# Kernel optimization log

Measured on AMD Instinct MI355X. Metric: run time of the kernel, lower is better.

## Reference

```python
import jax, jax.numpy as jnp
import numpy as np

N = 256
BIG = 1e9  # acts as +inf for float32 duals


def solve_lap(C):
    """Exact linear assignment (min-cost) via Jonker-Volgenant shortest
    augmenting paths with dual potentials. Returns [n,n] 0/1 labelling with
    exactly one 1 per row and per column (same optimum as scipy's
    linear_sum_assignment, up to ties)."""
    n = C.shape[0]
    dt = C.dtype
    big = jnp.asarray(BIG, dt)
    # 1-indexed padded cost: row/col 0 are dummies
    C1 = jnp.zeros((n + 1, n + 1), dt).at[1:, 1:].set(C)

    def row_body(i, carry):
        u, v, p = carry  # u: row duals, v: col duals, p[j] = row matched to col j (0 = free)
        p = p.at[0].set(i)

        def cond(st):
            u, v, p, used, minv, way, j0 = st
            return p[j0] != 0

        def body(st):
            u, v, p, used, minv, way, j0 = st
            used = used.at[j0].set(True)
            i0 = p[j0]
            cur = C1[i0] - u[i0] - v            # reduced costs of row i0, all cols
            upd = (~used) & (cur < minv)
            minv = jnp.where(upd, cur, minv)
            way = jnp.where(upd, j0, way)
            masked = jnp.where(used, big, minv)
            j1 = jnp.argmin(masked).astype(jnp.int32)
            delta = masked[j1]
            u = u.at[p].add(jnp.where(used, delta, jnp.asarray(0, dt)))
            v = v - jnp.where(used, delta, jnp.asarray(0, dt))
            minv = minv - jnp.where(used, jnp.asarray(0, dt), delta)
            return (u, v, p, used, minv, way, j1)

        used0 = jnp.zeros(n + 1, bool)
        minv0 = jnp.full(n + 1, big, dt)
        way0 = jnp.zeros(n + 1, jnp.int32)
        u, v, p, used, minv, way, j0 = jax.lax.while_loop(
            cond, body, (u, v, p, used0, minv0, way0, jnp.int32(0)))

        # augment along the alternating path back to the dummy column 0
        def acond(st):
            p_, j = st
            return j != 0

        def abody(st):
            p_, j = st
            j1 = way[j]
            p_ = p_.at[j].set(p_[j1])
            return (p_, j1)

        p, _ = jax.lax.while_loop(acond, abody, (p, j0))
        return (u, v, p)

    u0 = jnp.zeros(n + 1, dt)
    v0 = jnp.zeros(n + 1, dt)
    p0 = jnp.zeros(n + 1, jnp.int32)
    u, v, p = jax.lax.fori_loop(1, n + 1, row_body, (u0, v0, p0))

    rows = p[1:] - 1                      # row matched to each col (0-based)
    cols = jnp.arange(n)
    return jnp.zeros((n, n), dt).at[rows, cols].set(jnp.asarray(1.0, dt))


def setup_inputs() -> dict:
    key = jax.random.key(0)
    unaries = jax.random.normal(key, (N, N), dtype=jnp.float32)
    return {"unaries": unaries}


def reference(unaries):
    # LAPSolverModule.forward: exact min-cost assignment -> 0/1 labelling matrix
    return solve_lap(unaries)
```

## Files before the change

kernel.cpp:

```cpp
#include <hip/hip_runtime.h>

#define NN 256
#define BIGF 1e9f
#define NROWS_LDS 152
#define SMEM_BYTES (NROWS_LDS * 256 * 4)

template <int CTRL>
__device__ __forceinline__ float dpp_fmin(float x) {
    int t = __builtin_amdgcn_update_dpp(__float_as_int(x), __float_as_int(x),
                                        CTRL, 0xf, 0xf, false);
    return fminf(x, __int_as_float(t));
}

__device__ __forceinline__ float wave_min_bcast(float x) {
    x = dpp_fmin<0x111>(x);
    x = dpp_fmin<0x112>(x);
    x = dpp_fmin<0x114>(x);
    x = dpp_fmin<0x118>(x);
    x = dpp_fmin<0x142>(x);
    x = dpp_fmin<0x143>(x);
    return __int_as_float(__builtin_amdgcn_readlane(__float_as_int(x), 63));
}

extern "C" __global__ __launch_bounds__(64)
void lap_solve(const float* __restrict__ C, float* __restrict__ out) {
    extern __shared__ float rowc[];
    const int lane = threadIdx.x;
    const int base = lane * 4;
    const int boff = base * 4 - 1024;

    {
        const float4* src = (const float4*)C;
        float4*       dst = (float4*)rowc;
        #pragma unroll 8
        for (int idx = lane; idx < NROWS_LDS * 64; idx += 64) dst[idx] = src[idx];
    }
    __syncthreads();

    float v0 = 0.f, v1 = 0.f, v2 = 0.f, v3 = 0.f;
    float a0 = 0.f, a1 = 0.f, a2 = 0.f, a3 = 0.f;
    int   p0 = 0,  p1 = 0,  p2 = 0,  p3 = 0;

    float4 r = *(const float4*)((const char*)rowc + ((1 << 10) + boff));

    for (int i = 1; i <= NN; ++i) {
        float m0 = BIGF, m1 = BIGF, m2 = BIGF, m3 = BIGF;
        int   w0 = 0, w1 = 0, w2 = 0, w3 = 0;
        int   q0 = 0, q1 = 0, q2 = 0, q3 = 0;
        float ui = 0.0f;
        float u0 = 0.0f;
        int   j0 = 0, jF = 0;

        for (int guard = 0; guard < 300; ++guard) {
            float c0 = (r.x - u0) - v0;
            float c1 = (r.y - u0) - v1;
            float c2 = (r.z - u0) - v2;
            float c3 = (r.w - u0) - v3;
            if (!q0 && c0 < m0) { m0 = c0; w0 = j0; }
            if (!q1 && c1 < m1) { m1 = c1; w1 = j0; }
            if (!q2 && c2 < m2) { m2 = c2; w2 = j0; }
            if (!q3 && c3 < m3) { m3 = c3; w3 = j0; }

            float bv = fminf(fminf(m0, m1), fminf(m2, m3));
            int   bk = (m0 == bv) ? 0 : (m1 == bv) ? 1 : (m2 == bv) ? 2 : 3;
            int   rc = (bk == 0) ? p0 : (bk == 1) ? p1 : (bk == 2) ? p2 : p3;
            float ra = (bk == 0) ? a0 : (bk == 1) ? a1 : (bk == 2) ? a2 : a3;
            int   bj = base + bk + 1;
            int   rcs = rc << 10;

            float gmin = wave_min_bcast(bv);
            unsigned long long bal = __ballot(bv == gmin);
            int wl = (int)__builtin_ctzll(bal | 0x8000000000000000ULL);

            int rowoff = __builtin_amdgcn_readlane(rcs, wl);
            int ro = rowoff ? rowoff : 1024;
            float4 rn;
            if (ro <= NROWS_LDS * 1024)
                rn = *(const float4*)((const char*)rowc + (ro + boff));
            else
                rn = *(const float4*)((const char*)C + (ro + boff));

            int   j1  = __builtin_amdgcn_readlane(bj, wl);
            float u0n = __int_as_float(__builtin_amdgcn_readlane(__float_as_int(ra), wl));

            float delta = gmin;
            if (q0) { a0 += delta; v0 -= delta; } else { m0 -= delta; }
            if (q1) { a1 += delta; v1 -= delta; } else { m1 -= delta; }
            if (q2) { a2 += delta; v2 -= delta; } else { m2 -= delta; }
            if (q3) { a3 += delta; v3 -= delta; } else { m3 -= delta; }
            ui += delta;

            int oj = (j1 - 1) >> 2, sj = (j1 - 1) & 3;
            if (lane == oj) {
                if (sj == 0)      { q0 = 1; m0 = BIGF; }
                else if (sj == 1) { q1 = 1; m1 = BIGF; }
                else if (sj == 2) { q2 = 1; m2 = BIGF; }
                else              { q3 = 1; m3 = BIGF; }
            }

            j0 = j1; u0 = u0n; r = rn;
            if (rowoff == 0) { jF = j1; break; }
        }

        {
            int ni = (i < NN) ? (i + 1) : NN;
            int off = (ni << 10) + boff;
            if (ni <= NROWS_LDS) r = *(const float4*)((const char*)rowc + off);
            else                 r = *(const float4*)((const char*)C + off);
        }

        int j = jF;
        for (int g2 = 0; g2 < 300 && j != 0; ++g2) {
            int oj = (j - 1) >> 2, sj = (j - 1) & 3;
            int wsel = (sj == 0) ? w0 : (sj == 1) ? w1 : (sj == 2) ? w2 : w3;
            int jn = __builtin_amdgcn_readlane(wsel, oj);
            int pn; float an;
            if (jn == 0) { pn = i; an = ui; }
            else {
                int on = (jn - 1) >> 2, sn = (jn - 1) & 3;
                int   ps = (sn == 0) ? p0 : (sn == 1) ? p1 : (sn == 2) ? p2 : p3;
                float as = (sn == 0) ? a0 : (sn == 1) ? a1 : (sn == 2) ? a2 : a3;
                pn = __builtin_amdgcn_readlane(ps, on);
                an = __int_as_float(__builtin_amdgcn_readlane(__float_as_int(as), on));
            }
            if (lane == oj) {
                if (sj == 0)      { p0 = pn; a0 = an; }
                else if (sj == 1) { p1 = pn; a1 = an; }
                else if (sj == 2) { p2 = pn; a2 = an; }
                else              { p3 = pn; a3 = an; }
            }
            j = jn;
        }
    }

    if (p0) out[(p0 - 1) * NN + base + 0] = 1.0f;
    if (p1) out[(p1 - 1) * NN + base + 1] = 1.0f;
    if (p2) out[(p2 - 1) * NN + base + 2] = 1.0f;
    if (p3) out[(p3 - 1) * NN + base + 3] = 1.0f;
}

extern "C" void kernel_launch(void* const* d_in, const int* in_sizes, int n_in,
                              void* d_out, int out_size, void* d_ws, size_t ws_size,
                              hipStream_t stream) {
    const float* C   = (const float*)d_in[0];
    float*       out = (float*)d_out;

    static_assert(SMEM_BYTES <= 160 * 1024, "LDS budget");
    (void)hipFuncSetAttribute((const void*)lap_solve,
                              hipFuncAttributeMaxDynamicSharedMemorySize,
                              SMEM_BYTES);

    hipMemsetAsync(out, 0, NN * NN * sizeof(float), stream);
    lap_solve<<<dim3(1), dim3(64), SMEM_BYTES, stream>>>(C, out);
}
```

Before: 1.035 ms.

## Speculatively prefetch next cost row using previous row's search path history

Records the sequence of row offsets visited during each Dijkstra-style search in per-lane history registers. During the next row's search it speculatively loads the row predicted by that history before the argmin reduction finishes. If the actual next row matches the prediction, the prefetched data is used, which takes the LDS/global load off the serial dependency chain. The cost is an extra load on every iteration, more register pressure, and possible out-of-range speculative reads when the prediction is row 0; the gain depends on consecutive searches visiting the same rows in the same order.

```diff
diff --git a/kernel.cpp b/kernel.cpp
--- a/kernel.cpp
+++ b/kernel.cpp
@@ -4,6 +4,7 @@
 #define BIGF 1e9f
 #define NROWS_LDS 152
 #define SMEM_BYTES (NROWS_LDS * 256 * 4)
+#define LDS_LIMIT (NROWS_LDS * 1024)
 
 template <int CTRL>
 __device__ __forceinline__ float dpp_fmin(float x) {
@@ -41,6 +42,9 @@
     float a0 = 0.f, a1 = 0.f, a2 = 0.f, a3 = 0.f;
     int   p0 = 0,  p1 = 0,  p2 = 0,  p3 = 0;
 
+    int h0 = 0, h1 = 0, h2 = 0, h3 = 0, h4 = 0;
+    int g0 = 0, g1 = 0, g2 = 0, g3 = 0, g4 = 0;
+
     float4 r = *(const float4*)((const char*)rowc + ((1 << 10) + boff));
 
     for (int i = 1; i <= NN; ++i) {
@@ -52,6 +56,21 @@
         int   j0 = 0, jF = 0;
 
         for (int guard = 0; guard < 300; ++guard) {
+            const int t   = guard + 1;
+            const int seg = t >> 6, idx = t & 63;
+
+            int pred;
+            if (seg == 0)      pred = __builtin_amdgcn_readlane(h0, idx);
+            else if (seg == 1) pred = __builtin_amdgcn_readlane(h1, idx);
+            else if (seg == 2) pred = __builtin_amdgcn_readlane(h2, idx);
+            else if (seg == 3) pred = __builtin_amdgcn_readlane(h3, idx);
+            else               pred = __builtin_amdgcn_readlane(h4, idx);
+            float4 rpre;
+            if (pred <= LDS_LIMIT)
+                rpre = *(const float4*)((const char*)rowc + (pred + boff));
+            else
+                rpre = *(const float4*)((const char*)C + (pred + boff));
+
             float c0 = (r.x - u0) - v0;
             float c1 = (r.y - u0) - v1;
             float c2 = (r.z - u0) - v2;
@@ -73,12 +92,19 @@
             int wl = (int)__builtin_ctzll(bal | 0x8000000000000000ULL);
 
             int rowoff = __builtin_amdgcn_readlane(rcs, wl);
-            int ro = rowoff ? rowoff : 1024;
             float4 rn;
-            if (ro <= NROWS_LDS * 1024)
-                rn = *(const float4*)((const char*)rowc + (ro + boff));
+            if (rowoff == pred)
+                rn = rpre;
+            else if (rowoff <= LDS_LIMIT)
+                rn = *(const float4*)((const char*)rowc + (rowoff + boff));
             else
-                rn = *(const float4*)((const char*)C + (ro + boff));
+                rn = *(const float4*)((const char*)C + (rowoff + boff));
+
+            if (seg == 0)      { if (lane == idx) g0 = rowoff; }
+            else if (seg == 1) { if (lane == idx) g1 = rowoff; }
+            else if (seg == 2) { if (lane == idx) g2 = rowoff; }
+            else if (seg == 3) { if (lane == idx) g3 = rowoff; }
+            else               { if (lane == idx) g4 = rowoff; }
 
             int   j1  = __builtin_amdgcn_readlane(bj, wl);
             float u0n = __int_as_float(__builtin_amdgcn_readlane(__float_as_int(ra), wl));
@@ -102,6 +128,8 @@
             if (rowoff == 0) { jF = j1; break; }
         }
 
+        h0 = g0; h1 = g1; h2 = g2; h3 = g3; h4 = g4;
+
         {
             int ni = (i < NN) ? (i + 1) : NN;
             int off = (ni << 10) + boff;
@@ -110,7 +138,7 @@
         }
 
         int j = jF;
-        for (int g2 = 0; g2 < 300 && j != 0; ++g2) {
+        for (int g2w = 0; g2w < 300 && j != 0; ++g2w) {
             int oj = (j - 1) >> 2, sj = (j - 1) & 3;
             int wsel = (sj == 0) ? w0 : (sj == 1) ? w1 : (sj == 2) ? w2 : w3;
             int jn = __builtin_amdgcn_readlane(wsel, oj);
@@ -150,6 +178,6 @@
                               hipFuncAttributeMaxDynamicSharedMemorySize,
                               SMEM_BYTES);
 
-    hipMemsetAsync(out, 0, NN * NN * sizeof(float), stream);
+    (void)hipMemsetAsync(out, 0, NN * NN * sizeof(float), stream);
     lap_solve<<<dim3(1), dim3(64), SMEM_BYTES, stream>>>(C, out);
 }
```

Measured after the change: 1.454 ms. +40.5%, slower.
